# Kernel optimization log

Hardware: AMD Instinct MI355X
Metric: run time of the kernel (lower is better)

## Reference

```python
import jax, jax.numpy as jnp
import numpy as np

NUM_LESION_CLS = 8
MAX_INST = 64          # instance ids in mask_gt are < MAX_INST
SIZE_TH = 100.0
# merge_classes=[[1],...,[8]] -> zero-based groups [0..7] => identity merge


def setup_inputs() -> dict:
    key = jax.random.key(0)
    k1, k2, k3 = jax.random.split(key, 3)
    B, H, W, K = 32, 1024, 1024, 64
    pred_class = jax.random.normal(k1, (B, NUM_LESION_CLS), dtype=jnp.float32)
    mask_gt = jax.random.randint(k2, (B, H, W), 0, MAX_INST, dtype=jnp.int32)
    label_gt = jax.random.randint(k3, (B, K, 2), 0, 32, dtype=jnp.int64)
    return {"pred_class": pred_class, "mask_gt": mask_gt, "label_gt": label_gt}


def reference(pred_class, mask_gt, label_gt):
    # Per-sample histogram of instance-id pixel counts: [B, MAX_INST]
    inst_sizes = jax.vmap(lambda m: jnp.bincount(m.reshape(-1), length=MAX_INST))(mask_gt)
    inst_ids = label_gt[..., 0]            # [B, K]
    labels = label_gt[..., 1]              # [B, K]
    sizes = jnp.take_along_axis(inst_sizes, inst_ids, axis=1).astype(jnp.float32)  # [B, K]
    valid = (labels > 0) & (labels <= NUM_LESION_CLS)                              # [B, K]
    # scatter sizes into per-class counts: cnts[b, label-1] += size (if valid)
    onehot = jax.nn.one_hot(jnp.where(valid, labels - 1, 0), NUM_LESION_CLS,
                            dtype=jnp.float32) * valid[..., None].astype(jnp.float32)
    cnts = jnp.einsum('bk,bkc->bc', sizes, onehot)                                 # [B, C]
    # merge_classes is identity here, so class_label == cnts groups
    class_label = jnp.minimum(cnts / SIZE_TH, 1.0)
    # BCEWithLogitsLoss (mean reduction), numerically stable form
    x = pred_class
    loss = jnp.mean(jnp.maximum(x, 0.0) - x * class_label + jnp.log1p(jnp.exp(-jnp.abs(x))))
    return loss
```

## Files before the change

kernel.cpp:

```cpp
#include <hip/hip_runtime.h>
#include <math.h>

#define NB 32
#define HW (1024 * 1024)
#define BINS 64
#define KLBL 64
#define NCLS 8
#define BPI 64
#define TPB 256
#define CHUNK4 4096

__global__ __launch_bounds__(TPB) void hist_kernel(const int* __restrict__ mask,
                                                   int* __restrict__ hist) {
    __shared__ int sh[4][BINS];
    const int tid = threadIdx.x;
    const int b = blockIdx.x / BPI;
    const int part = blockIdx.x % BPI;
    const int wave = tid >> 6;

    sh[tid >> 6][tid & 63] = 0;
    __syncthreads();

    const int4* __restrict__ p4 =
        (const int4*)(mask + (size_t)b * HW) + (size_t)part * CHUNK4;

    #pragma unroll
    for (int h = 0; h < 2; ++h) {
        int4 v[8];
        #pragma unroll
        for (int k = 0; k < 8; ++k)
            v[k] = p4[(h * 8 + k) * TPB + tid];
        #pragma unroll
        for (int k = 0; k < 8; ++k) {
            atomicAdd(&sh[wave][v[k].x & 63], 1);
            atomicAdd(&sh[wave][v[k].y & 63], 1);
            atomicAdd(&sh[wave][v[k].z & 63], 1);
            atomicAdd(&sh[wave][v[k].w & 63], 1);
        }
    }
    __syncthreads();

    if (tid < BINS) {
        int s = sh[0][tid] + sh[1][tid] + sh[2][tid] + sh[3][tid];
        atomicAdd(&hist[b * BINS + tid], s);
    }
}

__global__ __launch_bounds__(TPB) void finalize_kernel(const float* __restrict__ pred,
                                                       const int* __restrict__ lg,
                                                       const int* __restrict__ hist,
                                                       float* __restrict__ out) {
    __shared__ float cnts[NB * NCLS];
    __shared__ float wsum[4];
    const int tid = threadIdx.x;

    cnts[tid] = 0.0f;
    __syncthreads();

    for (int e = tid; e < NB * KLBL; e += TPB) {
        int inst  = lg[e * 2 + 0];
        int label = lg[e * 2 + 1];
        if (label > 0 && label <= NCLS) {
            float sz = (float)hist[(e >> 6) * BINS + (inst & 63)];
            atomicAdd(&cnts[(e >> 6) * NCLS + (label - 1)], sz);
        }
    }
    __syncthreads();

    float x = pred[tid];
    float t = fminf(cnts[tid] * (1.0f / 100.0f), 1.0f);
    float l = fmaxf(x, 0.0f) - x * t + log1pf(expf(-fabsf(x)));

    for (int off = 32; off > 0; off >>= 1)
        l += __shfl_down(l, off, 64);
    if ((tid & 63) == 0) wsum[tid >> 6] = l;
    __syncthreads();
    if (tid == 0)
        out[0] = (wsum[0] + wsum[1] + wsum[2] + wsum[3]) * (1.0f / (NB * NCLS));
}

extern "C" void kernel_launch(void* const* d_in, const int* in_sizes, int n_in,
                              void* d_out, int out_size, void* d_ws, size_t ws_size,
                              hipStream_t stream) {
    const float* pred = (const float*)d_in[0];
    const int*   mask = (const int*)d_in[1];
    const int*   lg   = (const int*)d_in[2];
    float* out = (float*)d_out;
    int* hist = (int*)d_ws;

    hipMemsetAsync(hist, 0, NB * BINS * sizeof(int), stream);
    hist_kernel<<<NB * BPI, TPB, 0, stream>>>(mask, hist);
    finalize_kernel<<<1, TPB, 0, stream>>>(pred, lg, hist, out);
}
```

Before: 204.6 us.

## Replace LDS atomic histogram with wave ballot-based bit-match counting

Each lane now owns one bin. Each value is matched across the wavefront with six ballots on its id bits, and the lane adds the popcount of the matching mask instead of issuing an LDS atomicAdd per pixel. This removes shared-memory atomic contention. The cost is about 7 VALU/SALU operations per pixel, and the loads are split into smaller batches of 4 vectors with a launch-bounds occupancy hint. Because the bin id is masked to six bits, correctness holds only when ids are below 64, which the task guarantees.

```diff
diff --git a/kernel.cpp b/kernel.cpp
--- a/kernel.cpp
+++ b/kernel.cpp
@@ -10,36 +10,50 @@
 #define TPB 256
 #define CHUNK4 4096
 
-__global__ __launch_bounds__(TPB) void hist_kernel(const int* __restrict__ mask,
-                                                   int* __restrict__ hist) {
+typedef int v4i __attribute__((ext_vector_type(4)));
+
+__global__ __launch_bounds__(TPB, 8) void hist_kernel(const int* __restrict__ mask,
+                                                      int* __restrict__ hist) {
     __shared__ int sh[4][BINS];
     const int tid = threadIdx.x;
+    const int lane = tid & 63;
+    const int wave = tid >> 6;
     const int b = blockIdx.x / BPI;
     const int part = blockIdx.x % BPI;
-    const int wave = tid >> 6;
 
-    sh[tid >> 6][tid & 63] = 0;
-    __syncthreads();
+    unsigned long long ns[6];
+    #pragma unroll
+    for (int k = 0; k < 6; ++k)
+        ns[k] = ((lane >> k) & 1) ? 0ULL : ~0ULL;
 
-    const int4* __restrict__ p4 =
-        (const int4*)(mask + (size_t)b * HW) + (size_t)part * CHUNK4;
+    const v4i* __restrict__ p4 =
+        (const v4i*)(mask + (size_t)b * HW) + (size_t)part * CHUNK4;
 
+    unsigned cnt = 0;
     #pragma unroll
-    for (int h = 0; h < 2; ++h) {
-        int4 v[8];
+    for (int h = 0; h < 4; ++h) {
+        v4i v[4];
         #pragma unroll
-        for (int k = 0; k < 8; ++k)
-            v[k] = p4[(h * 8 + k) * TPB + tid];
+        for (int k = 0; k < 4; ++k)
+            v[k] = p4[(h * 4 + k) * TPB + tid];
         #pragma unroll
-        for (int k = 0; k < 8; ++k) {
-            atomicAdd(&sh[wave][v[k].x & 63], 1);
-            atomicAdd(&sh[wave][v[k].y & 63], 1);
-            atomicAdd(&sh[wave][v[k].z & 63], 1);
-            atomicAdd(&sh[wave][v[k].w & 63], 1);
+        for (int k = 0; k < 4; ++k) {
+            #pragma unroll
+            for (int c = 0; c < 4; ++c) {
+                int val = v[k][c];
+                unsigned long long m = ~0ULL;
+                #pragma unroll
+                for (int bit = 0; bit < 6; ++bit) {
+                    unsigned long long bb = __ballot(((val >> bit) & 1) != 0);
+                    m &= bb ^ ns[bit];
+                }
+                cnt += (unsigned)__popcll(m);
+            }
         }
     }
+
+    sh[wave][lane] = (int)cnt;
     __syncthreads();
-
     if (tid < BINS) {
         int s = sh[0][tid] + sh[1][tid] + sh[2][tid] + sh[3][tid];
         atomicAdd(&hist[b * BINS + tid], s);
```

After: 210.9 us. 3.0% more time.
